# Kernel optimization log

Measured on AMD Instinct MI355X. Metric: run time of the kernel, lower is better.

The kernel has to match this reference:

```python
import jax, jax.numpy as jnp
from jax import lax
import numpy as np

H = 32  # hidden_size

def setup_inputs() -> dict:
    key = jax.random.key(0)
    ks = jax.random.split(key, 7)
    B, T = 32, 16384
    s = 1.0 / np.sqrt(H)  # torch LSTM/Linear init scale
    x = jax.random.normal(ks[0], (B, T, 1), dtype=jnp.float32)
    W_ih = jax.random.uniform(ks[1], (4 * H, 1), jnp.float32, -s, s)
    W_hh = jax.random.uniform(ks[2], (4 * H, H), jnp.float32, -s, s)
    b_ih = jax.random.uniform(ks[3], (4 * H,), jnp.float32, -s, s)
    b_hh = jax.random.uniform(ks[4], (4 * H,), jnp.float32, -s, s)
    W_out = jax.random.uniform(ks[5], (1, H), jnp.float32, -s, s)
    b_out = jax.random.uniform(ks[6], (1,), jnp.float32, -s, s)
    return {"x": x, "W_ih": W_ih, "W_hh": W_hh, "b_ih": b_ih,
            "b_hh": b_hh, "W_out": W_out, "b_out": b_out}

def reference(x, W_ih, W_hh, b_ih, b_hh, W_out, b_out):
    B, T, _ = x.shape
    # Precompute input contribution to all gates once: (B, T, 4H)
    pre = jnp.einsum('bti,gi->btg', x, W_ih) + b_ih + b_hh

    def step(carry, p_t):
        h, c = carry
        gates = p_t + h @ W_hh.T  # (B, 4H), torch gate order i,f,g,o
        i, f, g, o = jnp.split(gates, 4, axis=-1)
        c = jax.nn.sigmoid(f) * c + jax.nn.sigmoid(i) * jnp.tanh(g)
        h = jax.nn.sigmoid(o) * jnp.tanh(c)
        return (h, c), h

    h0 = jnp.zeros((B, H), x.dtype)
    (_, _), hs = lax.scan(step, (h0, h0), jnp.swapaxes(pre, 0, 1))
    hs = jnp.swapaxes(hs, 0, 1)  # (B, T, H)
    return hs @ W_out.T + b_out  # (B, T, 1)
```

## Files before the change

### kernel.cpp

```cpp
#include <hip/hip_runtime.h>

#define T_LEN 16384
#define BATCH 32
#define HID 32
#define L2E 1.44269504088896340736f
#define SCLG (-2.0f * 1.44269504088896340736f)

typedef float f2 __attribute__((ext_vector_type(2)));
typedef unsigned u2_t __attribute__((ext_vector_type(2)));

#if __has_builtin(__builtin_amdgcn_exp2f)
#define EXP2F(x) __builtin_amdgcn_exp2f(x)
#else
#define EXP2F(x) __exp2f(x)
#endif
#if __has_builtin(__builtin_amdgcn_rcpf)
#define RCPF(x) __builtin_amdgcn_rcpf(x)
#else
#define RCPF(x) (1.0f / (x))
#endif

__device__ __forceinline__ float rlane(float v, int lane) {
    return __int_as_float(__builtin_amdgcn_readlane(__float_as_int(v), lane));
}

__device__ __forceinline__ float xhalf_lo_to_hi(float v) {
#if __has_builtin(__builtin_amdgcn_permlane32_swap)
    u2_t r = __builtin_amdgcn_permlane32_swap(__float_as_uint(v), __float_as_uint(v),
                                              false, false);
    return __uint_as_float(r.x);
#else
    return __shfl_xor(v, 32, 64);
#endif
}

__global__ __launch_bounds__(64) __attribute__((amdgpu_waves_per_eu(1, 1)))
void lstm_seq_kernel(const float* __restrict__ x,
                     const float* __restrict__ W_ih,
                     const float* __restrict__ W_hh,
                     const float* __restrict__ b_ih,
                     const float* __restrict__ b_hh,
                     const float* __restrict__ W_out,
                     const float* __restrict__ b_out,
                     float* __restrict__ out)
{
    const int b    = blockIdx.x;
    const int lane = threadIdx.x;
    const int j    = lane & 31;
    const bool upper = (lane >= 32);

    const int rowA = upper ? (32 + j) : j;
    const int rowB = upper ? (96 + j) : (64 + j);

    const float sclA = -L2E;
    const float sclB = upper ? -L2E : SCLG;

    f2 Wa2[16], Wb2[16];
    const f2* ra2 = reinterpret_cast<const f2*>(W_hh + (size_t)rowA * HID);
    const f2* rb2 = reinterpret_cast<const f2*>(W_hh + (size_t)rowB * HID);
    #pragma unroll
    for (int q = 0; q < 16; ++q) { Wa2[q] = ra2[q] * sclA; Wb2[q] = rb2[q] * sclB; }
    #pragma unroll
    for (int q = 0; q < 16; ++q) { asm("" : "+v"(Wa2[q]), "+v"(Wb2[q])); }

    const float wihA = sclA * W_ih[rowA];
    const float wihB = sclB * W_ih[rowB];
    const float bA = sclA * (b_ih[rowA] + b_hh[rowA]);
    const float bB = sclB * (b_ih[rowB] + b_hh[rowB]);

    const float wout = W_out[j];
    const float bout = b_out[0];

    __shared__ float phist[64 * 65];
    __shared__ float hbuf[64];

    float cS = 0.0f;
    hbuf[lane] = 0.0f;
    __syncthreads();

    const float* xb = x + (size_t)b * T_LEN;
    float*       yb = out + (size_t)b * T_LEN;
    const f2* hb2 = reinterpret_cast<const f2*>(&hbuf[32]);

    float xv = xb[lane];

    for (int t0 = 0; t0 < T_LEN; t0 += 64) {
        float xv_next = (t0 + 64 < T_LEN) ? xb[t0 + 64 + lane] : 0.0f;

        #pragma unroll 4
        for (int s = 0; s < 64; ++s) {
            const float xs  = rlane(xv, s);
            const float xpA = fmaf(xs, wihA, bA);
            const float xpB = fmaf(xs, wihB, bB);

            f2 hv2[16];
            #pragma unroll
            for (int p = 0; p < 16; ++p) hv2[p] = hb2[p];

            f2 zA[4], zB[4];
            zA[0].x = xpA; zA[0].y = 0.0f;
            zB[0].x = xpB; zB[0].y = 0.0f;
            #pragma unroll
            for (int p = 0; p < 16; ++p) {
                if (p == 0) {
                    asm("v_pk_fma_f32 %0, %1, %2, %0"
                        : "+v"(zA[0]) : "v"(hv2[0]), "v"(Wa2[0]));
                    asm("v_pk_fma_f32 %0, %1, %2, %0"
                        : "+v"(zB[0]) : "v"(hv2[0]), "v"(Wb2[0]));
                } else if (p < 4) {
                    asm("v_pk_mul_f32 %0, %1, %2"
                        : "=v"(zA[p]) : "v"(hv2[p]), "v"(Wa2[p]));
                    asm("v_pk_mul_f32 %0, %1, %2"
                        : "=v"(zB[p]) : "v"(hv2[p]), "v"(Wb2[p]));
                } else {
                    asm("v_pk_fma_f32 %0, %1, %2, %0"
                        : "+v"(zA[p & 3]) : "v"(hv2[p]), "v"(Wa2[p]));
                    asm("v_pk_fma_f32 %0, %1, %2, %0"
                        : "+v"(zB[p & 3]) : "v"(hv2[p]), "v"(Wb2[p]));
                }
            }
            const f2 rA = (zA[0] + zA[1]) + (zA[2] + zA[3]);
            const f2 rB = (zB[0] + zB[1]) + (zB[2] + zB[3]);
            const float za = rA.x + rA.y;
            const float zb = rB.x + rB.y;

            const float A = RCPF(1.0f + EXP2F(za));
            const float r = RCPF(1.0f + EXP2F(zb));
            const float tgS = fmaf(r, 2.0f * SCLG, -SCLG);
            const float so2 = r + r;

            const float up = A * tgS;
            const float tu = xhalf_lo_to_hi(up);

            cS = fmaf(A, cS, tu);
            const float r2 = RCPF(1.0f + EXP2F(cS));
            const float h  = fmaf(so2, r2, -r);

            hbuf[lane] = h;
            phist[s * 65 + lane] = h * wout;
        }

        __syncthreads();
        float acc = bout;
        #pragma unroll
        for (int k = 0; k < HID; ++k) acc += phist[lane * 65 + 32 + k];
        yb[t0 + lane] = acc;
        __syncthreads();

        xv = xv_next;
    }
}

extern "C" void kernel_launch(void* const* d_in, const int* in_sizes, int n_in,
                              void* d_out, int out_size, void* d_ws, size_t ws_size,
                              hipStream_t stream) {
    const float* x     = (const float*)d_in[0];
    const float* W_ih  = (const float*)d_in[1];
    const float* W_hh  = (const float*)d_in[2];
    const float* b_ih  = (const float*)d_in[3];
    const float* b_hh  = (const float*)d_in[4];
    const float* W_out = (const float*)d_in[5];
    const float* b_out = (const float*)d_in[6];
    float* out = (float*)d_out;

    lstm_seq_kernel<<<BATCH, 64, 0, stream>>>(x, W_ih, W_hh, b_ih, b_hh,
                                              W_out, b_out, out);
}
```

Baseline: 3.072 ms.

## Interleave two independent batch sequences per wavefront to hide recurrence latency

Each block now processes two batch rows, alternating their LSTM steps inside the time loop, and the grid shrinks from 32 to 16 blocks. The two independent dependency chains give the scheduler work to overlap the long serial latency of LDS round-trips, transcendental ops and cross-lane swaps. In exchange each wave issues twice the instructions per step, LDS use doubles, and fewer CUs are occupied, so per-step throughput rather than latency may become the limit.

After: 5.503 ms. 79.1% more time.

```diff
diff --git a/kernel.cpp b/kernel.cpp
--- a/kernel.cpp
+++ b/kernel.cpp
@@ -44,7 +44,7 @@
                      const float* __restrict__ b_out,
                      float* __restrict__ out)
 {
-    const int b    = blockIdx.x;
+    const int blk  = blockIdx.x;
     const int lane = threadIdx.x;
     const int j    = lane & 31;
     const bool upper = (lane >= 32);
@@ -71,83 +71,152 @@
     const float wout = W_out[j];
     const float bout = b_out[0];
 
-    __shared__ float phist[64 * 65];
-    __shared__ float hbuf[64];
-
-    float cS = 0.0f;
-    hbuf[lane] = 0.0f;
+    __shared__ float phistA[64 * 65];
+    __shared__ float phistB[64 * 65];
+    __shared__ float hbufA[64];
+    __shared__ float hbufB[64];
+
+    float cSA = 0.0f, cSB = 0.0f;
+    hbufA[lane] = 0.0f;
+    hbufB[lane] = 0.0f;
     __syncthreads();
 
-    const float* xb = x + (size_t)b * T_LEN;
-    float*       yb = out + (size_t)b * T_LEN;
-    const f2* hb2 = reinterpret_cast<const f2*>(&hbuf[32]);
-
-    float xv = xb[lane];
+    const float* xA = x + (size_t)(2 * blk) * T_LEN;
+    const float* xB = x + (size_t)(2 * blk + 1) * T_LEN;
+    float*       yA = out + (size_t)(2 * blk) * T_LEN;
+    float*       yB = out + (size_t)(2 * blk + 1) * T_LEN;
+
+    const f2* hb2A = reinterpret_cast<const f2*>(&hbufA[32]);
+    const f2* hb2B = reinterpret_cast<const f2*>(&hbufB[32]);
+
+    float xvA = xA[lane];
+    float xvB = xB[lane];
 
     for (int t0 = 0; t0 < T_LEN; t0 += 64) {
-        float xv_next = (t0 + 64 < T_LEN) ? xb[t0 + 64 + lane] : 0.0f;
-
-        #pragma unroll 4
+        float xvA_n = (t0 + 64 < T_LEN) ? xA[t0 + 64 + lane] : 0.0f;
+        float xvB_n = (t0 + 64 < T_LEN) ? xB[t0 + 64 + lane] : 0.0f;
+
+        #pragma unroll 2
         for (int s = 0; s < 64; ++s) {
-            const float xs  = rlane(xv, s);
-            const float xpA = fmaf(xs, wihA, bA);
-            const float xpB = fmaf(xs, wihB, bB);
-
-            f2 hv2[16];
+            {
+                const float xs  = rlane(xvA, s);
+                const float xpA = fmaf(xs, wihA, bA);
+                const float xpB = fmaf(xs, wihB, bB);
+
+                f2 hv2[16];
+                #pragma unroll
+                for (int p = 0; p < 16; ++p) hv2[p] = hb2A[p];
+
+                f2 zA[4], zB[4];
+                zA[0].x = xpA; zA[0].y = 0.0f;
+                zB[0].x = xpB; zB[0].y = 0.0f;
+                #pragma unroll
+                for (int p = 0; p < 16; ++p) {
+                    if (p == 0) {
+                        asm("v_pk_fma_f32 %0, %1, %2, %0"
+                            : "+v"(zA[0]) : "v"(hv2[0]), "v"(Wa2[0]));
+                        asm("v_pk_fma_f32 %0, %1, %2, %0"
+                            : "+v"(zB[0]) : "v"(hv2[0]), "v"(Wb2[0]));
+                    } else if (p < 4) {
+                        asm("v_pk_mul_f32 %0, %1, %2"
+                            : "=v"(zA[p]) : "v"(hv2[p]), "v"(Wa2[p]));
+                        asm("v_pk_mul_f32 %0, %1, %2"
+                            : "=v"(zB[p]) : "v"(hv2[p]), "v"(Wb2[p]));
+                    } else {
+                        asm("v_pk_fma_f32 %0, %1, %2, %0"
+                            : "+v"(zA[p & 3]) : "v"(hv2[p]), "v"(Wa2[p]));
+                        asm("v_pk_fma_f32 %0, %1, %2, %0"
+                            : "+v"(zB[p & 3]) : "v"(hv2[p]), "v"(Wb2[p]));
+                    }
+                }
+                const f2 rA = (zA[0] + zA[1]) + (zA[2] + zA[3]);
+                const f2 rB = (zB[0] + zB[1]) + (zB[2] + zB[3]);
+                const float za = rA.x + rA.y;
+                const float zb = rB.x + rB.y;
+
+                const float A = RCPF(1.0f + EXP2F(za));
+                const float r = RCPF(1.0f + EXP2F(zb));
+                const float tgS = fmaf(r, 2.0f * SCLG, -SCLG);
+                const float so2 = r + r;
+
+                const float up = A * tgS;
+                const float tu = xhalf_lo_to_hi(up);
+
+                cSA = fmaf(A, cSA, tu);
+                const float r2 = RCPF(1.0f + EXP2F(cSA));
+                const float h  = fmaf(so2, r2, -r);
+
+                hbufA[lane] = h;
+                phistA[s * 65 + lane] = h * wout;
+            }
+            {
+                const float xs  = rlane(xvB, s);
+                const float xpA = fmaf(xs, wihA, bA);
+                const float xpB = fmaf(xs, wihB, bB);
+
+                f2 hv2[16];
+                #pragma unroll
+                for (int p = 0; p < 16; ++p) hv2[p] = hb2B[p];
+
+                f2 zA[4], zB[4];
+                zA[0].x = xpA; zA[0].y = 0.0f;
+                zB[0].x = xpB; zB[0].y = 0.0f;
+                #pragma unroll
+                for (int p = 0; p < 16; ++p) {
+                    if (p == 0) {
+                        asm("v_pk_fma_f32 %0, %1, %2, %0"
+                            : "+v"(zA[0]) : "v"(hv2[0]), "v"(Wa2[0]));
+                        asm("v_pk_fma_f32 %0, %1, %2, %0"
+                            : "+v"(zB[0]) : "v"(hv2[0]), "v"(Wb2[0]));
+                    } else if (p < 4) {
+                        asm("v_pk_mul_f32 %0, %1, %2"
+                            : "=v"(zA[p]) : "v"(hv2[p]), "v"(Wa2[p]));
+                        asm("v_pk_mul_f32 %0, %1, %2"
+                            : "=v"(zB[p]) : "v"(hv2[p]), "v"(Wb2[p]));
+                    } else {
+                        asm("v_pk_fma_f32 %0, %1, %2, %0"
+                            : "+v"(zA[p & 3]) : "v"(hv2[p]), "v"(Wa2[p]));
+                        asm("v_pk_fma_f32 %0, %1, %2, %0"
+                            : "+v"(zB[p & 3]) : "v"(hv2[p]), "v"(Wb2[p]));
+                    }
+                }
+                const f2 rA = (zA[0] + zA[1]) + (zA[2] + zA[3]);
+                const f2 rB = (zB[0] + zB[1]) + (zB[2] + zB[3]);
+                const float za = rA.x + rA.y;
+                const float zb = rB.x + rB.y;
+
+                const float A = RCPF(1.0f + EXP2F(za));
+                const float r = RCPF(1.0f + EXP2F(zb));
+                const float tgS = fmaf(r, 2.0f * SCLG, -SCLG);
+                const float so2 = r + r;
+
+                const float up = A * tgS;
+                const float tu = xhalf_lo_to_hi(up);
+
+                cSB = fmaf(A, cSB, tu);
+                const float r2 = RCPF(1.0f + EXP2F(cSB));
+                const float h  = fmaf(so2, r2, -r);
+
+                hbufB[lane] = h;
+                phistB[s * 65 + lane] = h * wout;
+            }
+        }
+
+        __syncthreads();
+        {
+            float accA = bout, accB = bout;
             #pragma unroll
-            for (int p = 0; p < 16; ++p) hv2[p] = hb2[p];
-
-            f2 zA[4], zB[4];
-            zA[0].x = xpA; zA[0].y = 0.0f;
-            zB[0].x = xpB; zB[0].y = 0.0f;
-            #pragma unroll
-            for (int p = 0; p < 16; ++p) {
-                if (p == 0) {
-                    asm("v_pk_fma_f32 %0, %1, %2, %0"
-                        : "+v"(zA[0]) : "v"(hv2[0]), "v"(Wa2[0]));
-                    asm("v_pk_fma_f32 %0, %1, %2, %0"
-                        : "+v"(zB[0]) : "v"(hv2[0]), "v"(Wb2[0]));
-                } else if (p < 4) {
-                    asm("v_pk_mul_f32 %0, %1, %2"
-                        : "=v"(zA[p]) : "v"(hv2[p]), "v"(Wa2[p]));
-                    asm("v_pk_mul_f32 %0, %1, %2"
-                        : "=v"(zB[p]) : "v"(hv2[p]), "v"(Wb2[p]));
-                } else {
-                    asm("v_pk_fma_f32 %0, %1, %2, %0"
-                        : "+v"(zA[p & 3]) : "v"(hv2[p]), "v"(Wa2[p]));
-                    asm("v_pk_fma_f32 %0, %1, %2, %0"
-                        : "+v"(zB[p & 3]) : "v"(hv2[p]), "v"(Wb2[p]));
-                }
+            for (int k = 0; k < HID; ++k) {
+                accA += phistA[lane * 65 + 32 + k];
+                accB += phistB[lane * 65 + 32 + k];
             }
-            const f2 rA = (zA[0] + zA[1]) + (zA[2] + zA[3]);
-            const f2 rB = (zB[0] + zB[1]) + (zB[2] + zB[3]);
-            const float za = rA.x + rA.y;
-            const float zb = rB.x + rB.y;
-
-            const float A = RCPF(1.0f + EXP2F(za));
-            const float r = RCPF(1.0f + EXP2F(zb));
-            const float tgS = fmaf(r, 2.0f * SCLG, -SCLG);
-            const float so2 = r + r;
-
-            const float up = A * tgS;
-            const float tu = xhalf_lo_to_hi(up);
-
-            cS = fmaf(A, cS, tu);
-            const float r2 = RCPF(1.0f + EXP2F(cS));
-            const float h  = fmaf(so2, r2, -r);
-
-            hbuf[lane] = h;
-            phist[s * 65 + lane] = h * wout;
+            yA[t0 + lane] = accA;
+            yB[t0 + lane] = accB;
         }
-
         __syncthreads();
-        float acc = bout;
-        #pragma unroll
-        for (int k = 0; k < HID; ++k) acc += phist[lane * 65 + 32 + k];
-        yb[t0 + lane] = acc;
-        __syncthreads();
-
-        xv = xv_next;
+
+        xvA = xvA_n;
+        xvB = xvB_n;
     }
 }
 
@@ -163,6 +232,6 @@
     const float* b_out = (const float*)d_in[6];
     float* out = (float*)d_out;
 
-    lstm_seq_kernel<<<BATCH, 64, 0, stream>>>(x, W_ih, W_hh, b_ih, b_hh,
-                                              W_out, b_out, out);
-}
+    lstm_seq_kernel<<<BATCH / 2, 64, 0, stream>>>(x, W_ih, W_hh, b_ih, b_hh,
+                                                  W_out, b_out, out);
+}
```
